# Kernel optimization log

Hardware: AMD Instinct MI355X
Metric: run time of the kernel (lower is better)

## Reference

```python
import jax, jax.numpy as jnp
import numpy as np

D_MODEL = 1024
D_HEAD = 64
NHEADS = 8
IN_DIM = D_HEAD * NHEADS  # 512
EPS = 1e-5

def layernorm(x, g, b):
    mu = jnp.mean(x, axis=-1, keepdims=True)
    var = jnp.var(x, axis=-1, keepdims=True)
    return (x - mu) * jax.lax.rsqrt(var + EPS) * g + b

def setup_inputs() -> dict:
    key = jax.random.key(0)
    ks = jax.random.split(key, 8)
    B, M, L = 4, 8192, 64
    x = jax.random.normal(ks[0], (B, M, D_MODEL), dtype=jnp.float32)
    latents = jax.random.normal(ks[1], (B, L, D_MODEL), dtype=jnp.float32)
    s = 1.0 / np.sqrt(D_MODEL)
    Wq = jax.random.normal(ks[2], (D_MODEL, IN_DIM), dtype=jnp.float32) * s
    Wkv = jax.random.normal(ks[3], (D_MODEL, 2 * IN_DIM), dtype=jnp.float32) * s
    Wout = jax.random.normal(ks[4], (IN_DIM, D_MODEL), dtype=jnp.float32) * (1.0 / np.sqrt(IN_DIM))
    gm = jnp.ones((D_MODEL,), jnp.float32); bm = jnp.zeros((D_MODEL,), jnp.float32)
    gl = jnp.ones((D_MODEL,), jnp.float32); bl = jnp.zeros((D_MODEL,), jnp.float32)
    return {"x": x, "latents": latents, "Wq": Wq, "Wkv": Wkv, "Wout": Wout,
            "gm": gm, "bm": bm, "gl": gl, "bl": bl}

def reference(x, latents, Wq, Wkv, Wout, gm, bm, gl, bl):
    scale = D_HEAD ** (-0.5)
    xn = layernorm(x, gm, bm)            # [B, M, D]
    ln = layernorm(latents, gl, bl)      # [B, L, D]
    q = ln @ Wq                          # [B, L, IN_DIM]
    kv_input = jnp.concatenate([xn, ln], axis=-2)   # [B, M+L, D]
    kv = kv_input @ Wkv                  # [B, M+L, 2*IN_DIM]
    k, v = jnp.split(kv, 2, axis=-1)
    def heads(t):
        B, S, _ = t.shape
        return t.reshape(B, S, NHEADS, D_HEAD).transpose(0, 2, 1, 3)  # [B,H,S,dh]
    q, k, v = heads(q), heads(k), heads(v)
    q = q / scale  # NOTE: original divides by d_head**-0.5 (i.e. multiplies by sqrt(d_head))
    sim = jnp.einsum('bhid,bhjd->bhij', q, k)         # [B,H,L,M+L]
    sim = sim - jax.lax.stop_gradient(jnp.max(sim, axis=-1, keepdims=True))
    attn = jax.nn.softmax(sim, axis=-1)
    out = jnp.einsum('bhij,bhjd->bhid', attn, v)      # [B,H,L,dh]
    B, H, L, dh = out.shape
    out = out.transpose(0, 2, 1, 3).reshape(B, L, H * dh)
    return out @ Wout                                 # [B, L, D]
```

## Files before the change

kernel.cpp:

```cpp
#include <hip/hip_runtime.h>
#include <math.h>

#define DM 1024
#define INDIM 512
#define NH 8
#define DH 64
#define LQ 64
#define BATCH 4
#define MX 8192
#define SKV 8256
#define MROWS (BATCH * SKV)
#define NBH (BATCH * NH)
#define NT 258
#define NCHUNK 8
#define TPC 33

typedef _Float16 f16;
typedef f16 f16x8 __attribute__((ext_vector_type(8)));
typedef f16 f16x4 __attribute__((ext_vector_type(4)));
typedef float f32x4 __attribute__((ext_vector_type(4)));

typedef __attribute__((address_space(1))) const unsigned int gu32;
typedef __attribute__((address_space(3))) unsigned int lu32;
__device__ __forceinline__ void gload16(const f16* g, f16* l) {
    __builtin_amdgcn_global_load_lds((gu32*)g, (lu32*)l, 16, 0, 0);
}

__global__ __launch_bounds__(256) void ln_kernel(const float* __restrict__ src,
        const float* __restrict__ gam, const float* __restrict__ bet,
        f16* __restrict__ dst, f16* __restrict__ dst2,
        int rpb_in, int dst_off)
{
    int r = blockIdx.x;
    int tid = threadIdx.x;
    int b = r / rpb_in, m = r % rpb_in;
    const float4 v = *(const float4*)(src + (size_t)r * DM + tid * 4);
    float s = v.x + v.y + v.z + v.w;
    float q = v.x * v.x + v.y * v.y + v.z * v.z + v.w * v.w;
    for (int off = 32; off; off >>= 1) { s += __shfl_xor(s, off); q += __shfl_xor(q, off); }
    __shared__ float ps[4], pq[4];
    int w = tid >> 6;
    if ((tid & 63) == 0) { ps[w] = s; pq[w] = q; }
    __syncthreads();
    s = ps[0] + ps[1] + ps[2] + ps[3];
    q = pq[0] + pq[1] + pq[2] + pq[3];
    float mean = s * (1.f / DM);
    float var = q * (1.f / DM) - mean * mean;
    float rstd = rsqrtf(var + 1e-5f);
    const float4 gg = *(const float4*)(gam + tid * 4);
    const float4 bb = *(const float4*)(bet + tid * 4);
    f16x4 o;
    o[0] = (f16)((v.x - mean) * rstd * gg.x + bb.x);
    o[1] = (f16)((v.y - mean) * rstd * gg.y + bb.y);
    o[2] = (f16)((v.z - mean) * rstd * gg.z + bb.z);
    o[3] = (f16)((v.w - mean) * rstd * gg.w + bb.w);
    size_t drow = (size_t)b * SKV + dst_off + m;
    *(f16x4*)(dst + drow * DM + tid * 4) = o;
    if (dst2) *(f16x4*)(dst2 + (size_t)r * DM + tid * 4) = o;
}

__global__ __launch_bounds__(256) void transpose_w(const float* __restrict__ src,
        f16* __restrict__ dst, int R, int C, float scale)
{
    __shared__ float tile[32][33];
    int c0 = blockIdx.x * 32, r0 = blockIdx.y * 32;
    int tx = threadIdx.x & 31;
    int ty = threadIdx.x >> 5;
    #pragma unroll
    for (int k = 0; k < 4; k++)
        tile[ty + k * 8][tx] = src[(size_t)(r0 + ty + k * 8) * C + c0 + tx];
    __syncthreads();
    #pragma unroll
    for (int k = 0; k < 4; k++)
        dst[(size_t)(c0 + ty + k * 8) * R + r0 + tx] = (f16)(tile[tx][ty + k * 8] * scale);
}

template<int MODE>
__global__ __launch_bounds__(256) void gemm_bt(const f16* __restrict__ A, const f16* __restrict__ Bt,
        f16* __restrict__ Chi, f16* __restrict__ Clo,
        float* __restrict__ Cf, f16* __restrict__ vT,
        int M, int N, int K)
{
    __shared__ f16 As[128 * 32];
    __shared__ f16 Bs[128 * 32];
    int tid = threadIdx.x;
    int w = tid >> 6, l = tid & 63, l15 = l & 15, gq = l >> 4;
    int wr = w >> 1, wc = w & 1;
    int bm = blockIdx.x, bn = blockIdx.y;
    const f16* gA = A + (size_t)(bm * 128 + w * 32 + (l >> 2)) * K + (l & 3) * 8;
    const f16* gB = Bt + (size_t)(bn * 128 + w * 32 + (l >> 2)) * K + (l & 3) * 8;
    f16* lA0 = As + w * 1024;
    f16* lA1 = As + w * 1024 + 512;
    f16* lB0 = Bs + w * 1024;
    f16* lB1 = Bs + w * 1024 + 512;
    const size_t j1 = (size_t)16 * K;
    f32x4 acc[4][4] = {};
    for (int k0 = 0; k0 < K; k0 += 32) {
        __syncthreads();
        gload16(gA + k0, lA0);
        gload16(gA + k0 + j1, lA1);
        gload16(gB + k0, lB0);
        gload16(gB + k0 + j1, lB1);
        __syncthreads();
        f16x8 af[4], bfr[4];
        #pragma unroll
        for (int mm = 0; mm < 4; mm++)
            af[mm] = *(const f16x8*)&As[(wr * 64 + mm * 16 + l15) * 32 + gq * 8];
        #pragma unroll
        for (int nn = 0; nn < 4; nn++)
            bfr[nn] = *(const f16x8*)&Bs[(wc * 64 + nn * 16 + l15) * 32 + gq * 8];
        #pragma unroll
        for (int mm = 0; mm < 4; mm++)
            #pragma unroll
            for (int nn = 0; nn < 4; nn++)
                acc[mm][nn] = __builtin_amdgcn_mfma_f32_16x16x32_f16(af[mm], bfr[nn], acc[mm][nn], 0, 0, 0);
    }
    int rowb = bm * 128 + wr * 64 + gq * 4;
    int colb = bn * 128 + wc * 64 + l15;
    #pragma unroll
    for (int mm = 0; mm < 4; mm++)
    #pragma unroll
    for (int nn = 0; nn < 4; nn++)
    #pragma unroll
    for (int i = 0; i < 4; i++) {
        int row = rowb + mm * 16 + i;
        int col = colb + nn * 16;
        float v = acc[mm][nn][i];
        if (MODE == 1) {
            Cf[(size_t)row * N + col] = v;
        } else if (MODE == 3) {
            f16 hi = (f16)v;
            Chi[(size_t)row * N + col] = hi;
            Clo[(size_t)row * N + col] = (f16)(v - (float)hi);
        } else {
            if (col < INDIM) {
                f16 hi = (f16)v;
                Chi[(size_t)row * INDIM + col] = hi;
                Clo[(size_t)row * INDIM + col] = (f16)(v - (float)hi);
            } else {
                int b = row / SKV; int key = row - b * SKV;
                int hd = col - INDIM;
                vT[(size_t)((b * NH + (hd >> 6)) * DH + (hd & 63)) * SKV + key] = (f16)v;
            }
        }
    }
}

__global__ __launch_bounds__(512) void attn_kernel(const f16* __restrict__ q_hi, const f16* __restrict__ q_lo,
        const f16* __restrict__ k_hi, const f16* __restrict__ k_lo,
        const f16* __restrict__ vT,
        float* __restrict__ pO, float* __restrict__ pm, float* __restrict__ pl)
{
    __shared__ f16 P_lds[8][64][40];
    __shared__ float O_sum[64][64];
    __shared__ float m_lds[8][64];
    __shared__ float l_lds[8][64];
    int bh = blockIdx.x & (NBH - 1);
    int chunk = blockIdx.x >> 5;
    int b = bh >> 3, h = bh & 7;
    int cstart = chunk * TPC;
    int cend = cstart + TPC; if (cend > NT) cend = NT;
    int tid = threadIdx.x, w = tid >> 6, l = tid & 63, l15 = l & 15, gq = l >> 4;
    for (int i = tid; i < 64 * 64; i += 512) ((float*)O_sum)[i] = 0.f;
    f16x8 qfh[4][2], qfl[4][2];
    #pragma unroll
    for (int nb = 0; nb < 4; nb++)
        #pragma unroll
        for (int dh = 0; dh < 2; dh++) {
            size_t off = (size_t)(b * LQ + nb * 16 + l15) * INDIM + h * DH + dh * 32 + gq * 8;
            qfh[nb][dh] = *(const f16x8*)&q_hi[off];
            qfl[nb][dh] = *(const f16x8*)&q_lo[off];
        }
    const f16* kbh = k_hi + (size_t)b * SKV * INDIM + h * DH;
    const f16* kbl = k_lo + (size_t)b * SKV * INDIM + h * DH;
    const f16* vb = vT + (size_t)bh * DH * SKV;
    f32x4 accO[4][4] = {};
    float m_st[4] = {-1e30f, -1e30f, -1e30f, -1e30f};
    float l_st[4] = {0.f, 0.f, 0.f, 0.f};
    __syncthreads();
    for (int t = cstart + w; t < cend; t += 8) {
        int key0 = t * 32;
        f32x4 S[2][4] = {};
        f16x8 kah[2][2], kal[2][2];
        #pragma unroll
        for (int kbi = 0; kbi < 2; kbi++)
            #pragma unroll
            for (int dh = 0; dh < 2; dh++) {
                size_t off = (size_t)(key0 + kbi * 16 + l15) * INDIM + dh * 32 + gq * 8;
                kah[kbi][dh] = *(const f16x8*)&kbh[off];
                kal[kbi][dh] = *(const f16x8*)&kbl[off];
            }
        #pragma unroll
        for (int kbi = 0; kbi < 2; kbi++)
            #pragma unroll
            for (int nb = 0; nb < 4; nb++) {
                S[kbi][nb] = __builtin_amdgcn_mfma_f32_16x16x32_f16(kah[kbi][0], qfh[nb][0], S[kbi][nb], 0, 0, 0);
                S[kbi][nb] = __builtin_amdgcn_mfma_f32_16x16x32_f16(kah[kbi][1], qfh[nb][1], S[kbi][nb], 0, 0, 0);
                S[kbi][nb] = __builtin_amdgcn_mfma_f32_16x16x32_f16(kah[kbi][0], qfl[nb][0], S[kbi][nb], 0, 0, 0);
                S[kbi][nb] = __builtin_amdgcn_mfma_f32_16x16x32_f16(kah[kbi][1], qfl[nb][1], S[kbi][nb], 0, 0, 0);
                S[kbi][nb] = __builtin_amdgcn_mfma_f32_16x16x32_f16(kal[kbi][0], qfh[nb][0], S[kbi][nb], 0, 0, 0);
                S[kbi][nb] = __builtin_amdgcn_mfma_f32_16x16x32_f16(kal[kbi][1], qfh[nb][1], S[kbi][nb], 0, 0, 0);
            }
        #pragma unroll
        for (int nb = 0; nb < 4; nb++) {
            float tm = -1e30f;
            #pragma unroll
            for (int kbi = 0; kbi < 2; kbi++)
                #pragma unroll
                for (int i = 0; i < 4; i++) tm = fmaxf(tm, S[kbi][nb][i]);
            tm = fmaxf(tm, __shfl_xor(tm, 16));
            tm = fmaxf(tm, __shfl_xor(tm, 32));
            float nm = fmaxf(m_st[nb], tm);
            float corr = __expf(m_st[nb] - nm);
            m_st[nb] = nm;
            float rs = 0.f;
            #pragma unroll
            for (int kbi = 0; kbi < 2; kbi++) {
                f16x4 pk;
                #pragma unroll
                for (int i = 0; i < 4; i++) {
                    float p = __expf(S[kbi][nb][i] - nm);
                    rs += p;
                    pk[i] = (f16)p;
                }
                *(f16x4*)&P_lds[w][nb * 16 + l15][kbi * 16 + gq * 4] = pk;
            }
            rs += __shfl_xor(rs, 16);
            rs += __shfl_xor(rs, 32);
            l_st[nb] = l_st[nb] * corr + rs;
            #pragma unroll
            for (int db = 0; db < 4; db++) accO[db][nb] *= corr;
        }
        #pragma unroll
        for (int db = 0; db < 4; db++) {
            f16x8 va = *(const f16x8*)&vb[(size_t)(db * 16 + l15) * SKV + key0 + gq * 8];
            #pragma unroll
            for (int nb = 0; nb < 4; nb++) {
                f16x8 pb = *(const f16x8*)&P_lds[w][nb * 16 + l15][gq * 8];
                accO[db][nb] = __builtin_amdgcn_mfma_f32_16x16x32_f16(va, pb, accO[db][nb], 0, 0, 0);
            }
        }
    }
    if (gq == 0) {
        #pragma unroll
        for (int nb = 0; nb < 4; nb++) {
            m_lds[w][nb * 16 + l15] = m_st[nb];
            l_lds[w][nb * 16 + l15] = l_st[nb];
        }
    }
    __syncthreads();
    #pragma unroll
    for (int nb = 0; nb < 4; nb++) {
        int qrow = nb * 16 + l15;
        float Mx = -1e30f;
        #pragma unroll
        for (int ww = 0; ww < 8; ww++) Mx = fmaxf(Mx, m_lds[ww][qrow]);
        float f = __expf(m_st[nb] - Mx);
        #pragma unroll
        for (int db = 0; db < 4; db++)
            #pragma unroll
            for (int i = 0; i < 4; i++)
                atomicAdd(&O_sum[db * 16 + gq * 4 + i][qrow], accO[db][nb][i] * f);
    }
    __syncthreads();
    {
        int qrow = tid >> 3, d0 = (tid & 7) * 8;
        float Mx = -1e30f;
        #pragma unroll
        for (int ww = 0; ww < 8; ww++) Mx = fmaxf(Mx, m_lds[ww][qrow]);
        float Ls = 0.f;
        #pragma unroll
        for (int ww = 0; ww < 8; ww++) Ls += l_lds[ww][qrow] * __expf(m_lds[ww][qrow] - Mx);
        size_t base = ((size_t)(bh * NCHUNK + chunk) * 64 + qrow) * 64 + d0;
        float4 o0, o1;
        o0.x = O_sum[d0 + 0][qrow]; o0.y = O_sum[d0 + 1][qrow];
        o0.z = O_sum[d0 + 2][qrow]; o0.w = O_sum[d0 + 3][qrow];
        o1.x = O_sum[d0 + 4][qrow]; o1.y = O_sum[d0 + 5][qrow];
        o1.z = O_sum[d0 + 6][qrow]; o1.w = O_sum[d0 + 7][qrow];
        *(float4*)&pO[base] = o0;
        *(float4*)&pO[base + 4] = o1;
        if (d0 == 0) {
            pm[(bh * NCHUNK + chunk) * 64 + qrow] = Mx;
            pl[(bh * NCHUNK + chunk) * 64 + qrow] = Ls;
        }
    }
}

__global__ __launch_bounds__(256) void attn_merge(const float* __restrict__ pO,
        const float* __restrict__ pm, const float* __restrict__ pl, f16* __restrict__ attn_out)
{
    int bh = blockIdx.x; int b = bh >> 3, h = bh & 7;
    int tid = threadIdx.x;
    int row = tid >> 2, dseg = tid & 3;
    float pmv[NCHUNK];
    float mx = -1e30f;
    #pragma unroll
    for (int c = 0; c < NCHUNK; c++) {
        pmv[c] = pm[(bh * NCHUNK + c) * 64 + row];
        mx = fmaxf(mx, pmv[c]);
    }
    float L = 0.f;
    float wgt[NCHUNK];
    #pragma unroll
    for (int c = 0; c < NCHUNK; c++) {
        wgt[c] = __expf(pmv[c] - mx);
        L += pl[(bh * NCHUNK + c) * 64 + row] * wgt[c];
    }
    float inv = 1.f / L;
    float acc[16] = {};
    #pragma unroll
    for (int c = 0; c < NCHUNK; c++) {
        const float* p = &pO[((size_t)(bh * NCHUNK + c) * 64 + row) * 64 + dseg * 16];
        float wc = wgt[c];
        #pragma unroll
        for (int jj = 0; jj < 4; jj++) {
            float4 a = *(const float4*)(p + jj * 4);
            acc[jj * 4 + 0] += a.x * wc; acc[jj * 4 + 1] += a.y * wc;
            acc[jj * 4 + 2] += a.z * wc; acc[jj * 4 + 3] += a.w * wc;
        }
    }
    f16 o[16];
    #pragma unroll
    for (int j = 0; j < 16; j++) o[j] = (f16)(acc[j] * inv);
    f16* dst = &attn_out[(size_t)(b * LQ + row) * INDIM + h * DH + dseg * 16];
    *(f16x8*)dst = *(f16x8*)&o[0];
    *(f16x8*)(dst + 8) = *(f16x8*)&o[8];
}

extern "C" void kernel_launch(void* const* d_in, const int* in_sizes, int n_in,
                              void* d_out, int out_size, void* d_ws, size_t ws_size,
                              hipStream_t stream)
{
    const float* x    = (const float*)d_in[0];
    const float* lat  = (const float*)d_in[1];
    const float* Wq   = (const float*)d_in[2];
    const float* Wkv  = (const float*)d_in[3];
    const float* Wout = (const float*)d_in[4];
    const float* gm   = (const float*)d_in[5];
    const float* bm   = (const float*)d_in[6];
    const float* gl   = (const float*)d_in[7];
    const float* bl   = (const float*)d_in[8];
    float* out = (float*)d_out;

    char* ws = (char*)d_ws;
    size_t off = 0;
    auto alloc = [&](size_t bytes) {
        char* p = ws + off;
        off += (bytes + 255) & ~(size_t)255;
        return p;
    };
    f16* kv_in  = (f16*)alloc((size_t)MROWS * DM * 2);
    f16* k_hi   = (f16*)alloc((size_t)MROWS * INDIM * 2);
    f16* k_lo   = (f16*)alloc((size_t)MROWS * INDIM * 2);
    f16* vT     = (f16*)alloc((size_t)BATCH * NH * DH * SKV * 2);
    f16* q_in   = (f16*)alloc((size_t)BATCH * LQ * DM * 2);
    f16* q_hi   = (f16*)alloc((size_t)BATCH * LQ * INDIM * 2);
    f16* q_lo   = (f16*)alloc((size_t)BATCH * LQ * INDIM * 2);
    f16* wq_t   = (f16*)alloc((size_t)INDIM * DM * 2);
    f16* wkv_t  = (f16*)alloc((size_t)DM * DM * 2);
    f16* wout_t = (f16*)alloc((size_t)DM * INDIM * 2);
    f16* attn_o = (f16*)alloc((size_t)BATCH * LQ * INDIM * 2);
    float* pO   = (float*)kv_in;
    float* pm   = (float*)((char*)kv_in + (size_t)NBH * NCHUNK * 64 * 64 * 4);
    float* pl   = (float*)((char*)pm + (size_t)NBH * NCHUNK * 64 * 4);

    transpose_w<<<dim3(INDIM / 32, DM / 32), 256, 0, stream>>>(Wq, wq_t, DM, INDIM, 8.0f);
    transpose_w<<<dim3(DM / 32, DM / 32), 256, 0, stream>>>(Wkv, wkv_t, DM, DM, 1.0f);
    transpose_w<<<dim3(DM / 32, INDIM / 32), 256, 0, stream>>>(Wout, wout_t, INDIM, DM, 1.0f);
    ln_kernel<<<BATCH * MX, 256, 0, stream>>>(x, gm, bm, kv_in, nullptr, MX, 0);
    ln_kernel<<<BATCH * LQ, 256, 0, stream>>>(lat, gl, bl, kv_in, q_in, LQ, MX);
    gemm_bt<3><<<dim3(2, INDIM / 128), 256, 0, stream>>>(q_in, wq_t, q_hi, q_lo, nullptr, nullptr,
                                                         BATCH * LQ, INDIM, DM);
    gemm_bt<2><<<dim3(MROWS / 128, DM / 128), 256, 0, stream>>>(kv_in, wkv_t, k_hi, k_lo, nullptr, vT,
                                                                MROWS, DM, DM);
    attn_kernel<<<NBH * NCHUNK, 512, 0, stream>>>(q_hi, q_lo, k_hi, k_lo, vT, pO, pm, pl);
    attn_merge<<<NBH, 256, 0, stream>>>(pO, pm, pl, attn_o);
    gemm_bt<1><<<dim3(2, DM / 128), 256, 0, stream>>>(attn_o, wout_t, nullptr, nullptr, out, nullptr,
                                                      BATCH * LQ, DM, INDIM);
}
```

Baseline: 477.0 us.

## Double-buffer GEMM LDS tiles and swap grid order for A-tile reuse

The GEMM now keeps two LDS buffers and issues the global-to-LDS loads for the next K-slice before running the MFMAs on the current one. This removes one barrier per iteration and overlaps load latency with compute. The grid axes are also swapped so consecutive blocks share the same A row-tile across the N columns, which should improve L2 reuse of the large kv_in operand. LDS use doubles to 32KB per block, which may lower occupancy.

```diff
diff --git a/kernel.cpp b/kernel.cpp
--- a/kernel.cpp
+++ b/kernel.cpp
@@ -81,39 +81,43 @@
         float* __restrict__ Cf, f16* __restrict__ vT,
         int M, int N, int K)
 {
-    __shared__ f16 As[128 * 32];
-    __shared__ f16 Bs[128 * 32];
+    __shared__ f16 As[2][128 * 32];
+    __shared__ f16 Bs[2][128 * 32];
     int tid = threadIdx.x;
     int w = tid >> 6, l = tid & 63, l15 = l & 15, gq = l >> 4;
     int wr = w >> 1, wc = w & 1;
-    int bm = blockIdx.x, bn = blockIdx.y;
+    int bn = blockIdx.x, bm = blockIdx.y;
     const f16* gA = A + (size_t)(bm * 128 + w * 32 + (l >> 2)) * K + (l & 3) * 8;
     const f16* gB = Bt + (size_t)(bn * 128 + w * 32 + (l >> 2)) * K + (l & 3) * 8;
-    f16* lA0 = As + w * 1024;
-    f16* lA1 = As + w * 1024 + 512;
-    f16* lB0 = Bs + w * 1024;
-    f16* lB1 = Bs + w * 1024 + 512;
     const size_t j1 = (size_t)16 * K;
+    auto stage = [&](int buf, int k0) {
+        f16* lA = &As[buf][w * 1024];
+        f16* lB = &Bs[buf][w * 1024];
+        gload16(gA + k0, lA);
+        gload16(gA + k0 + j1, lA + 512);
+        gload16(gB + k0, lB);
+        gload16(gB + k0 + j1, lB + 512);
+    };
     f32x4 acc[4][4] = {};
+    stage(0, 0);
+    __syncthreads();
+    int cur = 0;
     for (int k0 = 0; k0 < K; k0 += 32) {
-        __syncthreads();
-        gload16(gA + k0, lA0);
-        gload16(gA + k0 + j1, lA1);
-        gload16(gB + k0, lB0);
-        gload16(gB + k0 + j1, lB1);
-        __syncthreads();
+        if (k0 + 32 < K) stage(cur ^ 1, k0 + 32);
         f16x8 af[4], bfr[4];
         #pragma unroll
         for (int mm = 0; mm < 4; mm++)
-            af[mm] = *(const f16x8*)&As[(wr * 64 + mm * 16 + l15) * 32 + gq * 8];
+            af[mm] = *(const f16x8*)&As[cur][(wr * 64 + mm * 16 + l15) * 32 + gq * 8];
         #pragma unroll
         for (int nn = 0; nn < 4; nn++)
-            bfr[nn] = *(const f16x8*)&Bs[(wc * 64 + nn * 16 + l15) * 32 + gq * 8];
+            bfr[nn] = *(const f16x8*)&Bs[cur][(wc * 64 + nn * 16 + l15) * 32 + gq * 8];
         #pragma unroll
         for (int mm = 0; mm < 4; mm++)
             #pragma unroll
             for (int nn = 0; nn < 4; nn++)
                 acc[mm][nn] = __builtin_amdgcn_mfma_f32_16x16x32_f16(af[mm], bfr[nn], acc[mm][nn], 0, 0, 0);
+        __syncthreads();
+        cur ^= 1;
     }
     int rowb = bm * 128 + wr * 64 + gq * 4;
     int colb = bn * 128 + wc * 64 + l15;
@@ -369,12 +373,12 @@
     transpose_w<<<dim3(DM / 32, INDIM / 32), 256, 0, stream>>>(Wout, wout_t, INDIM, DM, 1.0f);
     ln_kernel<<<BATCH * MX, 256, 0, stream>>>(x, gm, bm, kv_in, nullptr, MX, 0);
     ln_kernel<<<BATCH * LQ, 256, 0, stream>>>(lat, gl, bl, kv_in, q_in, LQ, MX);
-    gemm_bt<3><<<dim3(2, INDIM / 128), 256, 0, stream>>>(q_in, wq_t, q_hi, q_lo, nullptr, nullptr,
+    gemm_bt<3><<<dim3(INDIM / 128, 2), 256, 0, stream>>>(q_in, wq_t, q_hi, q_lo, nullptr, nullptr,
                                                          BATCH * LQ, INDIM, DM);
-    gemm_bt<2><<<dim3(MROWS / 128, DM / 128), 256, 0, stream>>>(kv_in, wkv_t, k_hi, k_lo, nullptr, vT,
+    gemm_bt<2><<<dim3(DM / 128, MROWS / 128), 256, 0, stream>>>(kv_in, wkv_t, k_hi, k_lo, nullptr, vT,
                                                                 MROWS, DM, DM);
     attn_kernel<<<NBH * NCHUNK, 512, 0, stream>>>(q_hi, q_lo, k_hi, k_lo, vT, pO, pm, pl);
     attn_merge<<<NBH, 256, 0, stream>>>(pO, pm, pl, attn_o);
-    gemm_bt<1><<<dim3(2, DM / 128), 256, 0, stream>>>(attn_o, wout_t, nullptr, nullptr, out, nullptr,
+    gemm_bt<1><<<dim3(DM / 128, 2), 256, 0, stream>>>(attn_o, wout_t, nullptr, nullptr, out, nullptr,
                                                       BATCH * LQ, DM, INDIM);
 }
```

Result: no change. 477.6 us (+0.1%).
